# Optimization experiments

Measured on AMD Instinct MI355X. Metric: run time of the kernel, lower is better.

## Reference

```python
import jax, jax.numpy as jnp
import numpy as np

N, E, D, H, C, L = 50000, 600000, 128, 128, 40, 2
NEG_SLOPE = 0.1


def setup_inputs() -> dict:
    key = jax.random.key(0)
    ks = jax.random.split(key, 12)

    def lin(k, din, dout):
        return (jax.random.normal(k, (din, dout), jnp.float32) / np.sqrt(din)).astype(jnp.float32)

    x = jax.random.normal(ks[0], (N, D), jnp.float32)
    edge_index = jax.random.randint(ks[1], (2, E), 0, N, dtype=jnp.int32)
    return {
        "x": x,
        "edge_index": edge_index,
        "enc_Wl": lin(ks[2], D, H),
        "enc_Wr": lin(ks[3], D, H),
        "enc_b": jnp.zeros((H,), jnp.float32),
        "lay_Wl": jnp.stack([lin(jax.random.fold_in(ks[4], i), H, H) for i in range(L)]),
        "lay_Wr": jnp.stack([lin(jax.random.fold_in(ks[5], i), H, H) for i in range(L)]),
        "lay_b": jnp.zeros((L, H), jnp.float32),
        "dec_Wl": lin(ks[6], H, C),
        "dec_Wr": lin(ks[7], H, C),
        "dec_b": jnp.zeros((C,), jnp.float32),
    }


def _sage(x, src, dst, inv_cnt, Wl, Wr, b):
    # mean-aggregate neighbor messages: gather x[src], scatter-sum to dst, divide by degree
    agg = jax.ops.segment_sum(x[src], dst, num_segments=N) * inv_cnt  # [N, d_in]
    return agg @ Wl + x @ Wr + b


def reference(x, edge_index, enc_Wl, enc_Wr, enc_b, lay_Wl, lay_Wr, lay_b, dec_Wl, dec_Wr, dec_b):
    src, dst = edge_index[0], edge_index[1]
    # in-degree per target node, clamped to 1 (PyG scatter-mean semantics: isolated nodes get 0)
    deg = jax.ops.segment_sum(jnp.ones((E,), jnp.float32), dst, num_segments=N)
    inv_cnt = (1.0 / jnp.maximum(deg, 1.0))[:, None]  # [N, 1]

    h = jax.nn.leaky_relu(_sage(x, src, dst, inv_cnt, enc_Wl, enc_Wr, enc_b), NEG_SLOPE)
    for i in range(L):
        h = jax.nn.leaky_relu(_sage(h, src, dst, inv_cnt, lay_Wl[i], lay_Wr[i], lay_b[i]), NEG_SLOPE)
    out = _sage(h, src, dst, inv_cnt, dec_Wl, dec_Wr, dec_b)
    return jax.nn.log_softmax(out, axis=1)
```

## Files before the change

### kernel.cpp

```cpp
#include <hip/hip_runtime.h>
#include <hip/hip_bf16.h>

#define NN 50000
#define EE 600000
#define HH 128
#define CC 40
#define NEG 0.1f
#define CAP 40

typedef __attribute__((ext_vector_type(8))) short bf16x8;
typedef __attribute__((ext_vector_type(4))) float f32x4;

__device__ __forceinline__ unsigned short f2bf(float f) {
    unsigned u = __float_as_uint(f);
    unsigned r = u + 0x7fffu + ((u >> 16) & 1u);
    return (unsigned short)(r >> 16);
}
__device__ __forceinline__ float bfhi(unsigned v) { return __uint_as_float(v & 0xFFFF0000u); }
__device__ __forceinline__ float bflo(unsigned v) { return __uint_as_float(v << 16); }

__global__ void k_build(const int* __restrict__ src, const int* __restrict__ dst,
                        int* __restrict__ counts, int* __restrict__ csr) {
    int t = blockIdx.x * blockDim.x + threadIdx.x;
    if (t < EE / 4) {
        int4 s4 = ((const int4*)src)[t];
        int4 d4 = ((const int4*)dst)[t];
        int sl;
        if ((unsigned)d4.x < (unsigned)NN) {
            sl = atomicAdd(&counts[d4.x], 1);
            if (sl < CAP) csr[d4.x * CAP + sl] = s4.x;
        }
        if ((unsigned)d4.y < (unsigned)NN) {
            sl = atomicAdd(&counts[d4.y], 1);
            if (sl < CAP) csr[d4.y * CAP + sl] = s4.y;
        }
        if ((unsigned)d4.z < (unsigned)NN) {
            sl = atomicAdd(&counts[d4.z], 1);
            if (sl < CAP) csr[d4.z * CAP + sl] = s4.z;
        }
        if ((unsigned)d4.w < (unsigned)NN) {
            sl = atomicAdd(&counts[d4.w], 1);
            if (sl < CAP) csr[d4.w * CAP + sl] = s4.w;
        }
    }
}

__global__ void k_xcast(const float* __restrict__ x, unsigned* __restrict__ xb) {
    int t = blockIdx.x * 256 + threadIdx.x;
    if (t < NN * HH / 4) {
        float4 v = ((const float4*)x)[t];
        uint2 o;
        o.x = ((unsigned)f2bf(v.y) << 16) | f2bf(v.x);
        o.y = ((unsigned)f2bf(v.w) << 16) | f2bf(v.z);
        ((uint2*)xb)[t] = o;
    }
}

struct SwzArgs {
    const float* src[8];
    unsigned short* dst[8];
};

template <int DOUT, int DOUTP>
__device__ __forceinline__ void swz_one(const float* __restrict__ W,
                                        unsigned short* __restrict__ dstf, int idx) {
    int k = idx / DOUTP, n = idx % DOUTP;
    unsigned short val = (n < DOUT) ? f2bf(W[k * DOUT + n]) : (unsigned short)0;
    int kt = k >> 5, kin = k & 31, nt = n >> 4, nin = n & 15;
    int lane = ((kin >> 3) << 4) | nin;
    int j = kin & 7;
    int NT = DOUTP >> 4;
    dstf[(((kt * NT + nt) * 64) + lane) * 8 + j] = val;
}

__global__ void k_swz_all(SwzArgs a) {
    int b = blockIdx.x;
    if (b < 384) {
        int which = b >> 6;
        int idx = (b & 63) * 256 + threadIdx.x;
        swz_one<HH, HH>(a.src[which], a.dst[which], idx);
    } else {
        int bb = b - 384;
        int which = 6 + bb / 24;
        int idx = (bb % 24) * 256 + threadIdx.x;
        swz_one<CC, 48>(a.src[which], a.dst[which], idx);
    }
}

__global__ __launch_bounds__(512) void k_layer(
    const unsigned short* __restrict__ hin,
    const int* __restrict__ counts, const int* __restrict__ csr,
    const unsigned short* __restrict__ B1f, const unsigned short* __restrict__ B2f,
    const float* __restrict__ bias, unsigned short* __restrict__ out) {
    __shared__ unsigned lds[16][72];
    int wid = threadIdx.x >> 6;
    int lane = threadIdx.x & 63;
    int m0 = blockIdx.x * 16;
    int g = lane & 7;
    int s = lane >> 3;
    const uint4* hw4 = (const uint4*)hin;

    int beg[2], cnt[2];
    float sc[2];
    int maxd = 0;
#pragma unroll
    for (int n = 0; n < 2; ++n) {
        int node = m0 + wid * 2 + n;
        int c = counts[node];
        c = c < CAP ? c : CAP;
        beg[n] = node * CAP;
        cnt[n] = c;
        sc[n] = 1.0f / (float)(c > 0 ? c : 1);
        maxd = maxd > c ? maxd : c;
    }
    int rounds = (maxd + 7) >> 3;

    for (int ph = 0; ph < 2; ++ph) {
        float acc[2][8];
#pragma unroll
        for (int n = 0; n < 2; ++n)
#pragma unroll
            for (int d = 0; d < 8; ++d) acc[n][d] = 0.f;

        uint4 v[2]; int ok[2];
        auto issue = [&](int r, uint4* vv, int* okk) {
#pragma unroll
            for (int n = 0; n < 2; ++n) {
                int idx = r * 8 + s;
                int o = idx < cnt[n];
                int row = csr[beg[n] + (o ? idx : 0)];
                vv[n] = hw4[(size_t)row * 16 + ph * 8 + g];
                okk[n] = o;
            }
        };
        if (rounds > 0) {
            issue(0, v, ok);
            for (int r = 0; r < rounds; ++r) {
                uint4 vn[2]; int okn[2];
                bool more = (r + 1 < rounds);
                if (more) issue(r + 1, vn, okn);
#pragma unroll
                for (int n = 0; n < 2; ++n) {
                    if (ok[n]) {
                        acc[n][0] += bflo(v[n].x); acc[n][1] += bfhi(v[n].x);
                        acc[n][2] += bflo(v[n].y); acc[n][3] += bfhi(v[n].y);
                        acc[n][4] += bflo(v[n].z); acc[n][5] += bfhi(v[n].z);
                        acc[n][6] += bflo(v[n].w); acc[n][7] += bfhi(v[n].w);
                    }
                }
                if (more) {
#pragma unroll
                    for (int n = 0; n < 2; ++n) { v[n] = vn[n]; ok[n] = okn[n]; }
                }
            }
        }
#pragma unroll
        for (int n = 0; n < 2; ++n) {
#pragma unroll
            for (int d = 0; d < 8; ++d) {
                float t = acc[n][d];
                t += __shfl_xor(t, 8, 64);
                t += __shfl_xor(t, 16, 64);
                t += __shfl_xor(t, 32, 64);
                acc[n][d] = t;
            }
            if (s == 0) {
                uint4 w4;
                w4.x = ((unsigned)f2bf(acc[n][1] * sc[n]) << 16) | f2bf(acc[n][0] * sc[n]);
                w4.y = ((unsigned)f2bf(acc[n][3] * sc[n]) << 16) | f2bf(acc[n][2] * sc[n]);
                w4.z = ((unsigned)f2bf(acc[n][5] * sc[n]) << 16) | f2bf(acc[n][4] * sc[n]);
                w4.w = ((unsigned)f2bf(acc[n][7] * sc[n]) << 16) | f2bf(acc[n][6] * sc[n]);
                *(uint4*)&lds[wid * 2 + n][ph * 32 + g * 4] = w4;
            }
        }
    }
    __syncthreads();

    int nin = lane & 15;
    int kq = lane >> 4;
    const unsigned* arow = &lds[nin][0];

    f32x4 acc1 = (f32x4){0.f, 0.f, 0.f, 0.f};

#pragma unroll
    for (int kt = 0; kt < 4; ++kt) {
        bf16x8 a1 = *(const bf16x8*)(arow + kt * 16 + kq * 4);
        bf16x8 a2 = *(const bf16x8*)(hin + (size_t)(m0 + nin) * HH + kt * 32 + kq * 8);
        bf16x8 b1 = *(const bf16x8*)(B1f + (((kt * 8 + wid) * 64) + lane) * 8);
        acc1 = __builtin_amdgcn_mfma_f32_16x16x32_bf16(a1, b1, acc1, 0, 0, 0);
        bf16x8 b2 = *(const bf16x8*)(B2f + (((kt * 8 + wid) * 64) + lane) * 8);
        acc1 = __builtin_amdgcn_mfma_f32_16x16x32_bf16(a2, b2, acc1, 0, 0, 0);
    }

    int col = wid * 16 + nin;
    float bv = bias[col];
#pragma unroll
    for (int r = 0; r < 4; ++r) {
        int m = m0 + kq * 4 + r;
        float v = acc1[r] + bv;
        v = fmaxf(v, NEG * v);
        out[(size_t)m * HH + col] = f2bf(v);
    }
}

__global__ __launch_bounds__(256) void k_pre(const unsigned short* __restrict__ h1,
                                             const unsigned short* __restrict__ Bf,
                                             unsigned short* __restrict__ t) {
    int wave = (blockIdx.x * 256 + threadIdx.x) >> 6;
    int lane = threadIdx.x & 63;
    int m0 = wave * 16;
    if (m0 >= NN) return;
    int nin = lane & 15, kq = lane >> 4;
    f32x4 acc[3];
#pragma unroll
    for (int j = 0; j < 3; ++j) acc[j] = (f32x4){0.f, 0.f, 0.f, 0.f};
#pragma unroll
    for (int kt = 0; kt < 4; ++kt) {
        bf16x8 a = *(const bf16x8*)(h1 + (size_t)(m0 + nin) * HH + kt * 32 + kq * 8);
#pragma unroll
        for (int j = 0; j < 3; ++j) {
            bf16x8 b = *(const bf16x8*)(Bf + (((kt * 3 + j) * 64) + lane) * 8);
            acc[j] = __builtin_amdgcn_mfma_f32_16x16x32_bf16(a, b, acc[j], 0, 0, 0);
        }
    }
#pragma unroll
    for (int j = 0; j < 3; ++j) {
        int col = j * 16 + nin;
#pragma unroll
        for (int r = 0; r < 4; ++r) {
            int m = m0 + kq * 4 + r;
            t[(size_t)m * 64 + col] = f2bf(acc[j][r]);
        }
    }
    int col2 = 48 + nin;
#pragma unroll
    for (int r = 0; r < 4; ++r) t[(size_t)(m0 + kq * 4 + r) * 64 + col2] = 0;
}

__global__ __launch_bounds__(256) void k_dec(
    const unsigned short* __restrict__ tbuf,
    const unsigned short* __restrict__ h1,
    const int* __restrict__ counts, const int* __restrict__ csr,
    const unsigned short* __restrict__ B2f, const float* __restrict__ bias,
    float* __restrict__ out) {
    __shared__ float aggT[16][52];
    int wid = threadIdx.x >> 6;
    int lane = threadIdx.x & 63;
    int m0 = blockIdx.x * 16;
    int g = lane & 7;
    int s = lane >> 3;
    const uint4* t4 = (const uint4*)tbuf;

    int beg[4], cnt[4];
    float sc[4];
    int maxd = 0;
#pragma unroll
    for (int n = 0; n < 4; ++n) {
        int node = m0 + wid * 4 + n;
        int c = counts[node];
        c = c < CAP ? c : CAP;
        beg[n] = node * CAP;
        cnt[n] = c;
        sc[n] = 1.0f / (float)(c > 0 ? c : 1);
        maxd = maxd > c ? maxd : c;
    }
    int rounds = (maxd + 7) >> 3;

    float acc[4][8];
#pragma unroll
    for (int n = 0; n < 4; ++n)
#pragma unroll
        for (int d = 0; d < 8; ++d) acc[n][d] = 0.f;

    uint4 v[4]; int ok[4];
    auto issue = [&](int r, uint4* vv, int* okk) {
#pragma unroll
        for (int n = 0; n < 4; ++n) {
            int idx = r * 8 + s;
            int o = idx < cnt[n];
            int row = csr[beg[n] + (o ? idx : 0)];
            vv[n] = t4[(size_t)row * 8 + g];
            okk[n] = o;
        }
    };
    if (rounds > 0) {
        issue(0, v, ok);
        for (int r = 0; r < rounds; ++r) {
            uint4 vn[4]; int okn[4];
            bool more = (r + 1 < rounds);
            if (more) issue(r + 1, vn, okn);
#pragma unroll
            for (int n = 0; n < 4; ++n) {
                if (ok[n]) {
                    acc[n][0] += bflo(v[n].x); acc[n][1] += bfhi(v[n].x);
                    acc[n][2] += bflo(v[n].y); acc[n][3] += bfhi(v[n].y);
                    acc[n][4] += bflo(v[n].z); acc[n][5] += bfhi(v[n].z);
                    acc[n][6] += bflo(v[n].w); acc[n][7] += bfhi(v[n].w);
                }
            }
            if (more) {
#pragma unroll
                for (int n = 0; n < 4; ++n) { v[n] = vn[n]; ok[n] = okn[n]; }
            }
        }
    }
#pragma unroll
    for (int n = 0; n < 4; ++n) {
#pragma unroll
        for (int d = 0; d < 8; ++d) {
            float t = acc[n][d];
            t += __shfl_xor(t, 8, 64);
            t += __shfl_xor(t, 16, 64);
            t += __shfl_xor(t, 32, 64);
            acc[n][d] = t;
        }
        if (s == 0 && g < 6) {
            float4 p0, p1;
            p0.x = acc[n][0] * sc[n]; p0.y = acc[n][1] * sc[n];
            p0.z = acc[n][2] * sc[n]; p0.w = acc[n][3] * sc[n];
            p1.x = acc[n][4] * sc[n]; p1.y = acc[n][5] * sc[n];
            p1.z = acc[n][6] * sc[n]; p1.w = acc[n][7] * sc[n];
            *(float4*)&aggT[wid * 4 + n][8 * g] = p0;
            *(float4*)&aggT[wid * 4 + n][8 * g + 4] = p1;
        }
    }
    __syncthreads();
    if (wid != 0) return;

    int nin = lane & 15, kq = lane >> 4;
    f32x4 acc2[3];
#pragma unroll
    for (int j = 0; j < 3; ++j) acc2[j] = (f32x4){0.f, 0.f, 0.f, 0.f};
#pragma unroll
    for (int kt = 0; kt < 4; ++kt) {
        bf16x8 a2 = *(const bf16x8*)(h1 + (size_t)(m0 + nin) * HH + kt * 32 + kq * 8);
#pragma unroll
        for (int j = 0; j < 3; ++j) {
            bf16x8 b2 = *(const bf16x8*)(B2f + (((kt * 3 + j) * 64) + lane) * 8);
            acc2[j] = __builtin_amdgcn_mfma_f32_16x16x32_bf16(a2, b2, acc2[j], 0, 0, 0);
        }
    }
    float bv[3];
#pragma unroll
    for (int t = 0; t < 3; ++t) {
        int col = t * 16 + nin;
        bv[t] = (col < CC) ? bias[col] : 0.f;
    }
#pragma unroll
    for (int r = 0; r < 4; ++r) {
        int m = m0 + kq * 4 + r;
        int ml = kq * 4 + r;
        float v[3];
        float mx = -1e30f;
#pragma unroll
        for (int t = 0; t < 3; ++t) {
            int col = t * 16 + nin;
            v[t] = acc2[t][r] + aggT[ml][col] + bv[t];
            if (col < CC) mx = fmaxf(mx, v[t]);
        }
        for (int off = 1; off < 16; off <<= 1) mx = fmaxf(mx, __shfl_xor(mx, off, 64));
        float sm = 0.f;
#pragma unroll
        for (int t = 0; t < 3; ++t) {
            int col = t * 16 + nin;
            if (col < CC) sm += expf(v[t] - mx);
        }
        for (int off = 1; off < 16; off <<= 1) sm += __shfl_xor(sm, off, 64);
        float lse = mx + logf(sm);
#pragma unroll
        for (int t = 0; t < 3; ++t) {
            int col = t * 16 + nin;
            if (col < CC) out[(size_t)m * CC + col] = v[t] - lse;
        }
    }
}

extern "C" void kernel_launch(void* const* d_in, const int* in_sizes, int n_in,
                              void* d_out, int out_size, void* d_ws, size_t ws_size,
                              hipStream_t stream) {
    const float* x      = (const float*)d_in[0];
    const int*   ei     = (const int*)d_in[1];
    const float* enc_Wl = (const float*)d_in[2];
    const float* enc_Wr = (const float*)d_in[3];
    const float* enc_b  = (const float*)d_in[4];
    const float* lay_Wl = (const float*)d_in[5];
    const float* lay_Wr = (const float*)d_in[6];
    const float* lay_b  = (const float*)d_in[7];
    const float* dec_Wl = (const float*)d_in[8];
    const float* dec_Wr = (const float*)d_in[9];
    const float* dec_b  = (const float*)d_in[10];
    float* out = (float*)d_out;

    const int* src = ei;
    const int* dst = ei + EE;

    char* p = (char*)d_ws;
    auto carve = [&](size_t bytes) {
        char* r = p;
        p += (bytes + 255) & ~(size_t)255;
        return r;
    };
    int*            counts = (int*)carve(NN * 4);
    int*            csr    = (int*)carve((size_t)NN * CAP * 4);
    unsigned short* h1     = (unsigned short*)carve((size_t)NN * HH * 2);
    unsigned short* h2     = (unsigned short*)carve((size_t)NN * HH * 2);
    unsigned short* wf[8];
    for (int i = 0; i < 6; ++i) wf[i] = (unsigned short*)carve(HH * HH * 2);
    wf[6] = (unsigned short*)carve(HH * 48 * 2);
    wf[7] = (unsigned short*)carve(HH * 48 * 2);

    {
        SwzArgs a;
        a.src[0] = enc_Wl; a.src[1] = enc_Wr;
        a.src[2] = lay_Wl; a.src[3] = lay_Wr;
        a.src[4] = lay_Wl + HH * HH; a.src[5] = lay_Wr + HH * HH;
        a.src[6] = dec_Wl; a.src[7] = dec_Wr;
        for (int i = 0; i < 8; ++i) a.dst[i] = wf[i];
        k_swz_all<<<432, 256, 0, stream>>>(a);
    }

    hipMemsetAsync(counts, 0, NN * 4, stream);
    int eblk4 = (EE / 4 + 255) / 256;
    k_build<<<eblk4, 256, 0, stream>>>(src, dst, counts, csr);

    k_xcast<<<(NN * HH / 4 + 255) / 256, 256, 0, stream>>>(x, (unsigned*)h2);

    const int FB = NN / 16;
    k_layer<<<FB, 512, 0, stream>>>(h2, counts, csr, wf[0], wf[1], enc_b,      h1);
    k_layer<<<FB, 512, 0, stream>>>(h1, counts, csr, wf[2], wf[3], lay_b,      h2);
    k_layer<<<FB, 512, 0, stream>>>(h2, counts, csr, wf[4], wf[5], lay_b + HH, h1);

    k_pre<<<(NN / 16 + 3) / 4, 256, 0, stream>>>(h1, wf[6], h2);
    k_dec<<<FB, 256, 0, stream>>>(h2, h1, counts, csr, wf[7], dec_b, out);
}
```

Before: 323.7 us.

## Fold counts zeroing into swizzle kernel, one edge per thread, wider decoder blocks

Zeroes the degree counts inside the weight-swizzle kernel so the separate memset launch goes away. The CSR build now handles one edge per thread instead of four, which spreads the atomics across more threads. The decoder kernel runs 512 threads per block with 8 waves each aggregating 2 nodes instead of 4 waves with 4 nodes, raising memory-level parallelism on the gather. The decoder's MFMA stage still uses only wave 0, so more waves per block sit idle during that phase.

```diff
diff --git a/kernel.cpp b/kernel.cpp
--- a/kernel.cpp
+++ b/kernel.cpp
@@ -21,26 +21,12 @@
 
 __global__ void k_build(const int* __restrict__ src, const int* __restrict__ dst,
                         int* __restrict__ counts, int* __restrict__ csr) {
-    int t = blockIdx.x * blockDim.x + threadIdx.x;
-    if (t < EE / 4) {
-        int4 s4 = ((const int4*)src)[t];
-        int4 d4 = ((const int4*)dst)[t];
-        int sl;
-        if ((unsigned)d4.x < (unsigned)NN) {
-            sl = atomicAdd(&counts[d4.x], 1);
-            if (sl < CAP) csr[d4.x * CAP + sl] = s4.x;
-        }
-        if ((unsigned)d4.y < (unsigned)NN) {
-            sl = atomicAdd(&counts[d4.y], 1);
-            if (sl < CAP) csr[d4.y * CAP + sl] = s4.y;
-        }
-        if ((unsigned)d4.z < (unsigned)NN) {
-            sl = atomicAdd(&counts[d4.z], 1);
-            if (sl < CAP) csr[d4.z * CAP + sl] = s4.z;
-        }
-        if ((unsigned)d4.w < (unsigned)NN) {
-            sl = atomicAdd(&counts[d4.w], 1);
-            if (sl < CAP) csr[d4.w * CAP + sl] = s4.w;
+    int e = blockIdx.x * blockDim.x + threadIdx.x;
+    if (e < EE) {
+        int d = dst[e];
+        if ((unsigned)d < (unsigned)NN) {
+            int sl = atomicAdd(&counts[d], 1);
+            if (sl < CAP) csr[d * CAP + sl] = src[e];
         }
     }
 }
@@ -59,6 +45,7 @@
 struct SwzArgs {
     const float* src[8];
     unsigned short* dst[8];
+    int* counts;
 };
 
 template <int DOUT, int DOUTP>
@@ -75,6 +62,8 @@
 
 __global__ void k_swz_all(SwzArgs a) {
     int b = blockIdx.x;
+    int tid = b * 256 + threadIdx.x;
+    if (tid < NN) a.counts[tid] = 0;
     if (b < 384) {
         int which = b >> 6;
         int idx = (b & 63) * 256 + threadIdx.x;
@@ -237,7 +226,7 @@
     for (int r = 0; r < 4; ++r) t[(size_t)(m0 + kq * 4 + r) * 64 + col2] = 0;
 }
 
-__global__ __launch_bounds__(256) void k_dec(
+__global__ __launch_bounds__(512) void k_dec(
     const unsigned short* __restrict__ tbuf,
     const unsigned short* __restrict__ h1,
     const int* __restrict__ counts, const int* __restrict__ csr,
@@ -251,12 +240,12 @@
     int s = lane >> 3;
     const uint4* t4 = (const uint4*)tbuf;
 
-    int beg[4], cnt[4];
-    float sc[4];
+    int beg[2], cnt[2];
+    float sc[2];
     int maxd = 0;
 #pragma unroll
-    for (int n = 0; n < 4; ++n) {
-        int node = m0 + wid * 4 + n;
+    for (int n = 0; n < 2; ++n) {
+        int node = m0 + wid * 2 + n;
         int c = counts[node];
         c = c < CAP ? c : CAP;
         beg[n] = node * CAP;
@@ -266,16 +255,16 @@
     }
     int rounds = (maxd + 7) >> 3;
 
-    float acc[4][8];
-#pragma unroll
-    for (int n = 0; n < 4; ++n)
+    float acc[2][8];
+#pragma unroll
+    for (int n = 0; n < 2; ++n)
 #pragma unroll
         for (int d = 0; d < 8; ++d) acc[n][d] = 0.f;
 
-    uint4 v[4]; int ok[4];
+    uint4 v[2]; int ok[2];
     auto issue = [&](int r, uint4* vv, int* okk) {
 #pragma unroll
-        for (int n = 0; n < 4; ++n) {
+        for (int n = 0; n < 2; ++n) {
             int idx = r * 8 + s;
             int o = idx < cnt[n];
             int row = csr[beg[n] + (o ? idx : 0)];
@@ -286,11 +275,11 @@
     if (rounds > 0) {
         issue(0, v, ok);
         for (int r = 0; r < rounds; ++r) {
-            uint4 vn[4]; int okn[4];
+            uint4 vn[2]; int okn[2];
             bool more = (r + 1 < rounds);
             if (more) issue(r + 1, vn, okn);
 #pragma unroll
-            for (int n = 0; n < 4; ++n) {
+            for (int n = 0; n < 2; ++n) {
                 if (ok[n]) {
                     acc[n][0] += bflo(v[n].x); acc[n][1] += bfhi(v[n].x);
                     acc[n][2] += bflo(v[n].y); acc[n][3] += bfhi(v[n].y);
@@ -300,12 +289,12 @@
             }
             if (more) {
 #pragma unroll
-                for (int n = 0; n < 4; ++n) { v[n] = vn[n]; ok[n] = okn[n]; }
-            }
-        }
-    }
-#pragma unroll
-    for (int n = 0; n < 4; ++n) {
+                for (int n = 0; n < 2; ++n) { v[n] = vn[n]; ok[n] = okn[n]; }
+            }
+        }
+    }
+#pragma unroll
+    for (int n = 0; n < 2; ++n) {
 #pragma unroll
         for (int d = 0; d < 8; ++d) {
             float t = acc[n][d];
@@ -320,8 +309,8 @@
             p0.z = acc[n][2] * sc[n]; p0.w = acc[n][3] * sc[n];
             p1.x = acc[n][4] * sc[n]; p1.y = acc[n][5] * sc[n];
             p1.z = acc[n][6] * sc[n]; p1.w = acc[n][7] * sc[n];
-            *(float4*)&aggT[wid * 4 + n][8 * g] = p0;
-            *(float4*)&aggT[wid * 4 + n][8 * g + 4] = p1;
+            *(float4*)&aggT[wid * 2 + n][8 * g] = p0;
+            *(float4*)&aggT[wid * 2 + n][8 * g + 4] = p1;
         }
     }
     __syncthreads();
@@ -416,12 +405,11 @@
         a.src[4] = lay_Wl + HH * HH; a.src[5] = lay_Wr + HH * HH;
         a.src[6] = dec_Wl; a.src[7] = dec_Wr;
         for (int i = 0; i < 8; ++i) a.dst[i] = wf[i];
+        a.counts = counts;
         k_swz_all<<<432, 256, 0, stream>>>(a);
     }
 
-    hipMemsetAsync(counts, 0, NN * 4, stream);
-    int eblk4 = (EE / 4 + 255) / 256;
-    k_build<<<eblk4, 256, 0, stream>>>(src, dst, counts, csr);
+    k_build<<<(EE + 255) / 256, 256, 0, stream>>>(src, dst, counts, csr);
 
     k_xcast<<<(NN * HH / 4 + 255) / 256, 256, 0, stream>>>(x, (unsigned*)h2);
 
@@ -431,5 +419,5 @@
     k_layer<<<FB, 512, 0, stream>>>(h2, counts, csr, wf[4], wf[5], lay_b + HH, h1);
 
     k_pre<<<(NN / 16 + 3) / 4, 256, 0, stream>>>(h1, wf[6], h2);
-    k_dec<<<FB, 256, 0, stream>>>(h2, h1, counts, csr, wf[7], dec_b, out);
-}
+    k_dec<<<FB, 512, 0, stream>>>(h2, h1, counts, csr, wf[7], dec_b, out);
+}
```

Result: faster. 303.0 us (-6.4%).
